# Optimization experiments

Measured on AMD Instinct MI355X. Metric: run time of the kernel, lower is better.

The kernel has to match this reference:

```python
import jax, jax.numpy as jnp
import numpy as np

EMBED = 512
H = 8
HD = EMBED // H           # 64
NUM_CLS = 4
WIN = 32                  # one-sided window radius
DIL = 1
WLEN = 2 * WIN + 1        # 65
CTX = NUM_CLS + WLEN      # 69
PATCH_LEN = 8192
B = 1
S = NUM_CLS + PATCH_LEN
THETA = 10000.0
COORD_HIGH = 100000.0
NEG = -1e30


def _rotate_half(x):
    # [..., x1, x2, ...] -> [..., -x2, x1, ...]
    x1 = x[..., 0::2]
    x2 = x[..., 1::2]
    return jnp.stack([-x2, x1], axis=-1).reshape(x.shape)


def _rope2d(x, coords):
    # x: (B,H,L,HD), coords: (B,L,2)
    half = HD // 2
    inv_freq = 1.0 / (THETA ** (jnp.arange(0, half, 2, dtype=jnp.float32) / half))  # (half//2,)
    xy = coords / COORD_HIGH
    fx = xy[..., 0][..., None] * inv_freq   # (B,L,half//2)
    fy = xy[..., 1][..., None] * inv_freq
    fx = jnp.repeat(fx, 2, axis=-1)         # (B,L,half)
    fy = jnp.repeat(fy, 2, axis=-1)
    freqs = jnp.concatenate([fx, fy], axis=-1)[:, None]  # (B,1,L,HD)
    return x * jnp.cos(freqs) + _rotate_half(x) * jnp.sin(freqs)


def setup_inputs() -> dict:
    key = jax.random.key(0)
    k1, k2, k3, k4, k5, k6 = jax.random.split(key, 6)
    x = jax.random.normal(k1, (B, S, EMBED), dtype=jnp.float32)
    coords = jax.random.uniform(k2, (B, PATCH_LEN, 2), dtype=jnp.float32) * COORD_HIGH
    sc = 1.0 / np.sqrt(EMBED)
    w_qkv = jax.random.normal(k3, (3 * EMBED, EMBED), dtype=jnp.float32) * sc
    b_qkv = jax.random.normal(k4, (3 * EMBED,), dtype=jnp.float32) * 0.02
    w_out = jax.random.normal(k5, (EMBED, EMBED), dtype=jnp.float32) * sc
    b_out = jax.random.normal(k6, (EMBED,), dtype=jnp.float32) * 0.02
    return {"x": x, "coords": coords, "w_qkv": w_qkv, "b_qkv": b_qkv,
            "w_out": w_out, "b_out": b_out}


def _forward(x, coords, w_qkv, b_qkv, w_out, b_out):
    Bb, seq_len, _ = x.shape
    qkv = x @ w_qkv.T + b_qkv                       # (B,S,3E)
    qkv = qkv.reshape(Bb, seq_len, 3, H, HD)
    qkv = jnp.transpose(qkv, (2, 0, 3, 1, 4))       # (3,B,H,S,HD)
    q, k, v = qkv[0], qkv[1], qkv[2]
    q_cls, k_cls, v_cls = q[:, :, :NUM_CLS], k[:, :, :NUM_CLS], v[:, :, :NUM_CLS]
    q_p, k_p, v_p = q[:, :, NUM_CLS:], k[:, :, NUM_CLS:], v[:, :, NUM_CLS:]

    q_p = _rope2d(q_p, coords)
    k_p = _rope2d(k_p, coords)
    k_all = jnp.concatenate([k_cls, k_p], axis=2)
    v_all = v

    scale = 1.0 / np.sqrt(HD)

    # --- global CLS attention: CLS queries attend to everything ---
    cls_scores = jnp.einsum('bhqd,bhkd->bhqk', q_cls, k_all) * scale
    cls_probs = jax.nn.softmax(cls_scores, axis=-1)
    cls_out = jnp.einsum('bhqk,bhkd->bhqd', cls_probs, v_all)

    # --- windowed patch attention: patch i -> [CLS | patches i-W..i+W (dilated)] ---
    L = PATCH_LEN
    pad = WIN * DIL
    k_pad = jnp.pad(k_p, ((0, 0), (0, 0), (pad, pad), (0, 0)))
    v_pad = jnp.pad(v_p, ((0, 0), (0, 0), (pad, pad), (0, 0)))
    gather_idx = jnp.arange(L)[:, None] + jnp.arange(WLEN)[None, :] * DIL  # (L,WLEN)
    k_win = k_pad[:, :, gather_idx]   # (B,H,L,WLEN,HD)
    v_win = v_pad[:, :, gather_idx]

    s_cls = jnp.einsum('bhld,bhcd->bhlc', q_p, k_cls) * scale     # (B,H,L,NUM_CLS)
    s_win = jnp.einsum('bhld,bhlwd->bhlw', q_p, k_win) * scale    # (B,H,L,WLEN)

    pos = jnp.arange(L)[:, None] + (jnp.arange(WLEN)[None, :] - WIN) * DIL
    in_bounds = (pos >= 0) & (pos < L)                            # (L,WLEN)
    s_win = jnp.where(in_bounds[None, None], s_win, NEG)

    scores = jnp.concatenate([s_cls, s_win], axis=-1)             # (B,H,L,CTX)
    probs = jax.nn.softmax(scores, axis=-1)
    p_cls, p_win = probs[..., :NUM_CLS], probs[..., NUM_CLS:]
    patch_out = (jnp.einsum('bhlc,bhcd->bhld', p_cls, v_cls)
                 + jnp.einsum('bhlw,bhlwd->bhld', p_win, v_win))

    out = jnp.concatenate([cls_out, patch_out], axis=2)           # (B,H,S,HD)
    out = jnp.transpose(out, (0, 2, 1, 3)).reshape(Bb, seq_len, EMBED)
    return out @ w_out.T + b_out


def reference(x, coords, w_qkv, b_qkv, w_out, b_out):
    return _forward(x, coords, w_qkv, b_qkv, w_out, b_out)
```

## Files before the change

kernel.cpp:

```cpp
#include <hip/hip_runtime.h>
#include <math.h>

#define EMBED 512
#define NHEAD 8
#define HD 64
#define NUM_CLS 4
#define WIN 32
#define WLEN 65
#define PATCH_LEN 8192
#define S_TOT 8196
#define QKV_LD 1536
#define VT_LD 8200

typedef short bf16x8 __attribute__((ext_vector_type(8)));
typedef float f32x4 __attribute__((ext_vector_type(4)));

__device__ __forceinline__ unsigned short f2bf(float f) {
    unsigned u = __float_as_uint(f);
    return (unsigned short)((u + 0x7fffu + ((u >> 16) & 1u)) >> 16);
}
__device__ __forceinline__ float bf2f(unsigned short v) {
    return __uint_as_float((unsigned)v << 16);
}

__global__ __launch_bounds__(256) void cast_all(const float* __restrict__ x,
                                                const float* __restrict__ wq,
                                                const float* __restrict__ wo,
                                                unsigned short* __restrict__ xb,
                                                unsigned short* __restrict__ wqb,
                                                unsigned short* __restrict__ wob)
{
    const int n1 = S_TOT * EMBED;
    const int n2 = 3 * EMBED * EMBED;
    const int n3 = EMBED * EMBED;
    const int i = (blockIdx.x * 256 + threadIdx.x) * 4;
    const float* src;
    unsigned short* dst;
    int j;
    if (i < n1)           { src = x;  dst = xb;  j = i; }
    else if (i < n1 + n2) { src = wq; dst = wqb; j = i - n1; }
    else if (i < n1 + n2 + n3) { src = wo; dst = wob; j = i - n1 - n2; }
    else return;
    const float4 v = *(const float4*)(src + j);
    ushort4 o;
    o.x = f2bf(v.x); o.y = f2bf(v.y); o.z = f2bf(v.z); o.w = f2bf(v.w);
    *(ushort4*)(dst + j) = o;
}

template <int MODE, typename OutT>
__global__ __launch_bounds__(256) void gemm_bf16_nt(const unsigned short* __restrict__ A,
                                                    const unsigned short* __restrict__ B,
                                                    const float* __restrict__ bias,
                                                    OutT* __restrict__ C,
                                                    int M, int N, int K,
                                                    const float* __restrict__ coords,
                                                    unsigned short* __restrict__ vT)
{
    __shared__ __align__(16) unsigned short As[128 * 32];
    __shared__ __align__(16) unsigned short Bs[128 * 32];
    const int tid = threadIdx.x;
    const int lane = tid & 63, w = tid >> 6;
    const int bn = blockIdx.x, bm = blockIdx.y;

    const int ar0 = tid >> 2;
    const int col8 = (tid & 3) * 8;
    int gm0 = bm * 128 + ar0;       if (gm0 >= M) gm0 = M - 1;
    int gm1 = bm * 128 + ar0 + 64;  if (gm1 >= M) gm1 = M - 1;
    const int gn0 = bn * 128 + ar0;
    const int gn1 = bn * 128 + ar0 + 64;
    const unsigned short* pa0 = A + (size_t)gm0 * K + col8;
    const unsigned short* pa1 = A + (size_t)gm1 * K + col8;
    const unsigned short* pb0 = B + (size_t)gn0 * K + col8;
    const unsigned short* pb1 = B + (size_t)gn1 * K + col8;
    unsigned short* la0 = As + tid * 8;
    unsigned short* la1 = As + (tid + 256) * 8;
    unsigned short* lb0 = Bs + tid * 8;
    unsigned short* lb1 = Bs + (tid + 256) * 8;

    const int wr = (w & 1) * 64;
    const int wc = (w >> 1) * 64;
    const int fr = lane & 15;
    const int fk = (lane >> 4) * 8;

    f32x4 acc[4][4];
#pragma unroll
    for (int mi = 0; mi < 4; ++mi)
#pragma unroll
        for (int ni = 0; ni < 4; ++ni) acc[mi][ni] = (f32x4)0.f;

    for (int k0 = 0; k0 < K; k0 += 32) {
        __builtin_amdgcn_global_load_lds((const __attribute__((address_space(1))) void*)(pa0 + k0),
                                         (__attribute__((address_space(3))) void*)la0, 16, 0, 0);
        __builtin_amdgcn_global_load_lds((const __attribute__((address_space(1))) void*)(pa1 + k0),
                                         (__attribute__((address_space(3))) void*)la1, 16, 0, 0);
        __builtin_amdgcn_global_load_lds((const __attribute__((address_space(1))) void*)(pb0 + k0),
                                         (__attribute__((address_space(3))) void*)lb0, 16, 0, 0);
        __builtin_amdgcn_global_load_lds((const __attribute__((address_space(1))) void*)(pb1 + k0),
                                         (__attribute__((address_space(3))) void*)lb1, 16, 0, 0);
        __syncthreads();

        bf16x8 af[4], bf[4];
#pragma unroll
        for (int mi = 0; mi < 4; ++mi)
            af[mi] = *(const bf16x8*)(As + (wr + mi * 16 + fr) * 32 + fk);
#pragma unroll
        for (int ni = 0; ni < 4; ++ni)
            bf[ni] = *(const bf16x8*)(Bs + (wc + ni * 16 + fr) * 32 + fk);
#pragma unroll
        for (int mi = 0; mi < 4; ++mi)
#pragma unroll
            for (int ni = 0; ni < 4; ++ni)
                acc[mi][ni] = __builtin_amdgcn_mfma_f32_16x16x32_bf16(af[mi], bf[ni], acc[mi][ni], 0, 0, 0);
        __syncthreads();
    }

    const int ccol = bn * 128 + wc + fr;

    if constexpr (MODE == 0) {
#pragma unroll
        for (int mi = 0; mi < 4; ++mi) {
            const int rbase = bm * 128 + wr + mi * 16 + (lane >> 4) * 4;
#pragma unroll
            for (int r = 0; r < 4; ++r) {
                const int row = rbase + r;
                if (row < M) {
#pragma unroll
                    for (int ni = 0; ni < 4; ++ni)
                        C[(size_t)row * N + ccol + ni * 16] = acc[mi][ni][r] + bias[ccol + ni * 16];
                }
            }
        }
    } else {
        __shared__ __align__(16) unsigned short EX[64 * 136];
        if (bn < 8) {
            ushort2* rt = (ushort2*)EX;
            for (int idx = tid; idx < 4096; idx += 256) {
                const int rr = idx >> 5, pr = idx & 31;
                int l = bm * 128 + rr - NUM_CLS;
                l = l < 0 ? 0 : (l > PATCH_LEN - 1 ? PATCH_LEN - 1 : l);
                const float cxy = coords[l * 2 + (pr >> 4)] * 1e-5f;
                const float f = cxy * __expf(-(float)(pr & 15) * 0.5756462732485114f);
                float sn, cs;
                __sincosf(f, &sn, &cs);
                ushort2 e; e.x = f2bf(cs); e.y = f2bf(sn);
                rt[idx] = e;
            }
            __syncthreads();
#pragma unroll
            for (int mi = 0; mi < 4; ++mi) {
                const int rloc0 = wr + mi * 16 + (lane >> 4) * 4;
#pragma unroll
                for (int r = 0; r < 4; ++r) {
                    const int rloc = rloc0 + r;
                    const int row = bm * 128 + rloc;
                    const bool patch = (row >= NUM_CLS) && (row < M);
#pragma unroll
                    for (int ni = 0; ni < 4; ++ni) {
                        const int col = ccol + ni * 16;
                        const float biased = acc[mi][ni][r] + bias[col];
                        const float prt = __shfl_xor(biased, 1);
                        float outv = biased;
                        if (patch) {
                            const ushort2 e = rt[rloc * 32 + ((col & 63) >> 1)];
                            const float cs = bf2f(e.x), sn = bf2f(e.y);
                            outv = (col & 1) ? (biased * cs + prt * sn)
                                             : (biased * cs - prt * sn);
                        }
                        if (row < M) C[(size_t)row * N + col] = (OutT)f2bf(outv);
                    }
                }
            }
        } else {
            const int dbase = (bn - 8) * 128;
#pragma unroll
            for (int mi = 0; mi < 4; ++mi) {
                const int rbase = bm * 128 + wr + mi * 16 + (lane >> 4) * 4;
#pragma unroll
                for (int ni = 0; ni < 4; ++ni) {
                    const int col = ccol + ni * 16;
#pragma unroll
                    for (int r = 0; r < 4; ++r) {
                        const int row = rbase + r;
                        if (row < M)
                            C[(size_t)row * N + col] = (OutT)f2bf(acc[mi][ni][r] + bias[col]);
                    }
                }
            }
            for (int p = 0; p < 2; ++p) {
                __syncthreads();
                if ((w >> 1) == p) {
#pragma unroll
                    for (int mi = 0; mi < 4; ++mi) {
                        const int tok0 = wr + mi * 16 + (lane >> 4) * 4;
                        const int rw = bm * 128 + tok0;
#pragma unroll
                        for (int ni = 0; ni < 4; ++ni) {
                            const int col = ccol + ni * 16;
                            const int dloc = fr + 16 * ni;
                            ushort4 o;
                            o.x = (rw + 0 < M) ? f2bf(acc[mi][ni][0] + bias[col]) : (unsigned short)0;
                            o.y = (rw + 1 < M) ? f2bf(acc[mi][ni][1] + bias[col]) : (unsigned short)0;
                            o.z = (rw + 2 < M) ? f2bf(acc[mi][ni][2] + bias[col]) : (unsigned short)0;
                            o.w = (rw + 3 < M) ? f2bf(acc[mi][ni][3] + bias[col]) : (unsigned short)0;
                            *(ushort4*)(EX + dloc * 136 + tok0) = o;
                        }
                    }
                }
                __syncthreads();
                const int d = tid >> 2;
                const int tch = (tid & 3) * 32;
                const int gtok = bm * 128 + tch;
                unsigned short* dst = vT + (size_t)(dbase + p * 64 + d) * VT_LD + gtok;
                const unsigned short* srcl = EX + d * 136 + tch;
                if (gtok + 32 <= VT_LD) {
#pragma unroll
                    for (int c2 = 0; c2 < 32; c2 += 8)
                        *(bf16x8*)(dst + c2) = *(const bf16x8*)(srcl + c2);
                } else {
                    for (int c2 = 0; c2 < 32; ++c2)
                        if (gtok + c2 < VT_LD) dst[c2] = srcl[c2];
                }
            }
        }
    }
}

#define CCH 128
#define NCHUNK ((S_TOT + CCH - 1) / CCH)
#define PSTRIDE 68

__global__ __launch_bounds__(256) void cls_attn_partial(const unsigned short* __restrict__ qkv,
                                                        float* __restrict__ part)
{
    const int h = blockIdx.x;
    const int c = blockIdx.y;
    const int tid = threadIdx.x;
    const int base = c * CCH;

    __shared__ float qs[4][64];
    __shared__ __align__(16) unsigned short Kl[128 * 64];
    __shared__ float sc[4][CCH];
    __shared__ float ored[4][4][64];
    __shared__ float ml[4][2];

    {
        const int qi = tid >> 6, d = tid & 63;
        qs[qi][d] = bf2f(qkv[(size_t)qi * QKV_LD + h * HD + d]);
    }
    for (int i = tid; i < 1024; i += 256) {
        const int kr = i >> 3;
        const int dc = (i & 7) ^ (kr & 7);
        int j = base + kr; if (j > S_TOT - 1) j = S_TOT - 1;
        const unsigned short* g = qkv + (size_t)j * QKV_LD + EMBED + h * HD + dc * 8;
        __builtin_amdgcn_global_load_lds((const __attribute__((address_space(1))) void*)g,
                                         (__attribute__((address_space(3))) void*)(Kl + i * 8), 16, 0, 0);
    }
    __syncthreads();

    {
        const int jj = tid & 127;
        const int qp = (tid >> 7) * 2;
        const int j = base + jj;
        float s0 = -INFINITY, s1 = -INFINITY;
        if (j < S_TOT) {
            float a0 = 0.f, a1 = 0.f;
#pragma unroll
            for (int cch = 0; cch < 8; ++cch) {
                const int slot = cch ^ (jj & 7);
                const bf16x8 kv8 = *(const bf16x8*)(Kl + jj * 64 + slot * 8);
#pragma unroll
                for (int u = 0; u < 8; ++u) {
                    const float kf = bf2f((unsigned short)kv8[u]);
                    a0 += qs[qp + 0][cch * 8 + u] * kf;
                    a1 += qs[qp + 1][cch * 8 + u] * kf;
                }
            }
            s0 = a0 * 0.125f; s1 = a1 * 0.125f;
        }
        sc[qp + 0][jj] = s0;
        sc[qp + 1][jj] = s1;
    }
    __syncthreads();

    const int w = tid >> 6, lane = tid & 63;
    {
        float m = fmaxf(sc[w][lane], sc[w][lane + 64]);
#pragma unroll
        for (int off = 32; off > 0; off >>= 1) m = fmaxf(m, __shfl_xor(m, off, 64));
        const float e0 = expf(sc[w][lane] - m);
        const float e1 = expf(sc[w][lane + 64] - m);
        sc[w][lane] = e0; sc[w][lane + 64] = e1;
        float lsum = e0 + e1;
#pragma unroll
        for (int off = 32; off > 0; off >>= 1) lsum += __shfl_xor(lsum, off, 64);
        if (lane == 0) { ml[w][0] = m; ml[w][1] = lsum; }
    }
    __syncthreads();

    {
        const int g = w, d = lane;
        float a0 = 0.f, a1 = 0.f, a2 = 0.f, a3 = 0.f;
        for (int jj = g; jj < CCH; jj += 4) {
            const int j = base + jj;
            if (j >= S_TOT) break;
            const float vv = bf2f(qkv[(size_t)j * QKV_LD + 2 * EMBED + h * HD + d]);
            a0 += sc[0][jj] * vv; a1 += sc[1][jj] * vv;
            a2 += sc[2][jj] * vv; a3 += sc[3][jj] * vv;
        }
        ored[g][0][d] = a0; ored[g][1][d] = a1; ored[g][2][d] = a2; ored[g][3][d] = a3;
    }
    __syncthreads();

    {
        const int qi = tid >> 6, d = tid & 63;
        const float o = ored[0][qi][d] + ored[1][qi][d] + ored[2][qi][d] + ored[3][qi][d];
        float* pb = part + ((size_t)(h * NCHUNK + c) * 4 + qi) * PSTRIDE;
        pb[d] = o;
        if (d == 0) { pb[64] = ml[qi][0]; pb[65] = ml[qi][1]; }
    }
}

__global__ __launch_bounds__(256) void cls_attn_combine(const float* __restrict__ part,
                                                        unsigned short* __restrict__ attn)
{
    const int h = blockIdx.x;
    const int qi = threadIdx.x >> 6, d = threadIdx.x & 63;
    float M = -INFINITY;
    for (int c = 0; c < NCHUNK; ++c)
        M = fmaxf(M, part[((size_t)(h * NCHUNK + c) * 4 + qi) * PSTRIDE + 64]);
    float acc = 0.f, L = 0.f;
    for (int c = 0; c < NCHUNK; ++c) {
        const float* pb = part + ((size_t)(h * NCHUNK + c) * 4 + qi) * PSTRIDE;
        const float s = expf(pb[64] - M);
        acc += s * pb[d];
        L   += s * pb[65];
    }
    attn[(size_t)qi * EMBED + h * HD + d] = f2bf(acc / L);
}

#define SW 116
#define PW 136

__global__ __launch_bounds__(256) void patch_attn_mfma(
    const unsigned short* __restrict__ qkv,
    const unsigned short* __restrict__ vT,
    unsigned short* __restrict__ attnb)
{
    const int l0 = blockIdx.x * 32;
    const int h = blockIdx.y;
    const int tid = threadIdx.x;
    const int lane = tid & 63, w = tid >> 6;

    __shared__ __align__(16) unsigned short Qs[32 * 64];
    __shared__ __align__(16) unsigned short Ks[112 * 64];
    __shared__ __align__(16) unsigned short Vt[64 * 128];
    __shared__ __align__(16) float Sm[32 * SW];

    {
        const int i = tid;
        const int t = i >> 3;
        const int dcl = (i & 7) ^ (t & 7);
        const unsigned short* g = qkv + (size_t)(NUM_CLS + l0 + t) * QKV_LD + h * HD + dcl * 8;
        __builtin_amdgcn_global_load_lds((const __attribute__((address_space(1))) void*)g,
                                         (__attribute__((address_space(3))) void*)(Qs + i * 8), 16, 0, 0);
    }
    for (int i = tid; i < 896; i += 256) {
        const int c = i >> 3;
        const int dcl = (i & 7) ^ (c & 7);
        int tok = (c >= 104 && c < 108) ? (c - 104) : (l0 - 32 + c);
        tok = tok < 0 ? 0 : (tok > S_TOT - 1 ? S_TOT - 1 : tok);
        const unsigned short* g = qkv + (size_t)tok * QKV_LD + EMBED + h * HD + dcl * 8;
        __builtin_amdgcn_global_load_lds((const __attribute__((address_space(1))) void*)g,
                                         (__attribute__((address_space(3))) void*)(Ks + i * 8), 16, 0, 0);
    }
    for (int i = tid; i < 1024; i += 256) {
        const int d = i >> 4;
        const int kcl = (i & 15) ^ (d & 15);
        const int c0 = kcl * 8;
        int tokb = (c0 == 104) ? 0 : (l0 - 32 + c0);
        tokb = tokb < 0 ? 0 : (tokb > 8192 ? 8192 : tokb);
        const unsigned short* g = vT + (size_t)(h * HD + d) * VT_LD + tokb;
        __builtin_amdgcn_global_load_lds((const __attribute__((address_space(1))) void*)g,
                                         (__attribute__((address_space(3))) void*)(Vt + i * 8), 16, 0, 0);
    }
    __syncthreads();

    bf16x8 qf[2][2];
#pragma unroll
    for (int mt = 0; mt < 2; ++mt)
#pragma unroll
        for (int ks = 0; ks < 2; ++ks) {
            const int row = mt * 16 + (lane & 15);
            const int dc = (ks * 4 + (lane >> 4)) ^ (row & 7);
            qf[mt][ks] = *(const bf16x8*)(Qs + row * 64 + dc * 8);
        }
    for (int idx = w; idx < 14; idx += 4) {
        const int mt = idx & 1, nt = idx >> 1;
        f32x4 acc = (f32x4)0.f;
#pragma unroll
        for (int ks = 0; ks < 2; ++ks) {
            const int kr = nt * 16 + (lane & 15);
            const int dc = (ks * 4 + (lane >> 4)) ^ (kr & 7);
            const bf16x8 kf = *(const bf16x8*)(Ks + kr * 64 + dc * 8);
            acc = __builtin_amdgcn_mfma_f32_16x16x32_bf16(qf[mt][ks], kf, acc, 0, 0, 0);
        }
        const int col = nt * 16 + (lane & 15);
        const int r0 = mt * 16 + (lane >> 4) * 4;
#pragma unroll
        for (int r = 0; r < 4; ++r) Sm[(r0 + r) * SW + col] = acc[r];
    }
    __syncthreads();

    {
        const int t = tid >> 3, lq = tid & 7;
        float e[14];
        float m = -INFINITY;
#pragma unroll
        for (int j = 0; j < 14; ++j) {
            const int c = lq + 8 * j;
            bool valid;
            if (c >= 104) valid = (c < 108);
            else {
                const int r = c - 4;
                const int pos = l0 - 32 + r;
                valid = (c >= 4) && (c < 100) && (r >= t) && (r <= t + 64) &&
                        (pos >= 0) && (pos < PATCH_LEN);
            }
            e[j] = valid ? Sm[t * SW + c] * 0.125f : -INFINITY;
            m = fmaxf(m, e[j]);
        }
#pragma unroll
        for (int off = 1; off < 8; off <<= 1) m = fmaxf(m, __shfl_xor(m, off, 64));
        float sum = 0.f;
#pragma unroll
        for (int j = 0; j < 14; ++j) { e[j] = expf(e[j] - m); sum += e[j]; }
#pragma unroll
        for (int off = 1; off < 8; off <<= 1) sum += __shfl_xor(sum, off, 64);
        const float inv = 1.f / sum;
        __syncthreads();
        unsigned short* P = (unsigned short*)Sm;
#pragma unroll
        for (int j = 0; j < 14; ++j) P[t * PW + lq + 8 * j] = f2bf(e[j] * inv);
        ushort2 z; z.x = 0; z.y = 0;
        *(ushort2*)(P + (tid >> 3) * PW + 112 + (tid & 7) * 2) = z;
    }
    __syncthreads();

    {
        const unsigned short* P = (const unsigned short*)Sm;
        const int mt = w & 1;
        bf16x8 pf[4];
#pragma unroll
        for (int ks = 0; ks < 4; ++ks) {
            const int row = mt * 16 + (lane & 15);
            pf[ks] = *(const bf16x8*)(P + row * PW + ks * 32 + (lane >> 4) * 8);
        }
#pragma unroll
        for (int nn = 0; nn < 2; ++nn) {
            const int nt = (w >> 1) + nn * 2;
            f32x4 acc = (f32x4)0.f;
#pragma unroll
            for (int ks = 0; ks < 4; ++ks) {
                const int d = nt * 16 + (lane & 15);
                const int kc = (ks * 4 + (lane >> 4)) ^ (d & 15);
                const bf16x8 vf = *(const bf16x8*)(Vt + d * 128 + kc * 8);
                acc = __builtin_amdgcn_mfma_f32_16x16x32_bf16(pf[ks], vf, acc, 0, 0, 0);
            }
            const int dcol = nt * 16 + (lane & 15);
            const int r0 = mt * 16 + (lane >> 4) * 4;
#pragma unroll
            for (int r = 0; r < 4; ++r)
                attnb[(size_t)(NUM_CLS + l0 + r0 + r) * EMBED + h * HD + dcol] = f2bf(acc[r]);
        }
    }
}

extern "C" void kernel_launch(void* const* d_in, const int* in_sizes, int n_in,
                              void* d_out, int out_size, void* d_ws, size_t ws_size,
                              hipStream_t stream)
{
    const float* x      = (const float*)d_in[0];
    const float* coords = (const float*)d_in[1];
    const float* w_qkv  = (const float*)d_in[2];
    const float* b_qkv  = (const float*)d_in[3];
    const float* w_out  = (const float*)d_in[4];
    const float* b_out  = (const float*)d_in[5];
    float* out = (float*)d_out;

    char* p = (char*)d_ws;
    unsigned short* qkv   = (unsigned short*)p;  p += (size_t)S_TOT * QKV_LD * 2;
    unsigned short* vT    = (unsigned short*)p;  p += (size_t)EMBED * VT_LD * 2;
    unsigned short* attnb = (unsigned short*)p;  p += (size_t)S_TOT * EMBED * 2;
    float*          part  = (float*)p;           p += (size_t)NHEAD * NCHUNK * 4 * PSTRIDE * 4;
    unsigned short* wob   = (unsigned short*)p;  p += (size_t)EMBED * EMBED * 2;
    unsigned short* xb    = (unsigned short*)p;  p += (size_t)S_TOT * EMBED * 2;
    unsigned short* wqb   = (unsigned short*)p;


    {
        const int total = S_TOT * EMBED + 3 * EMBED * EMBED + EMBED * EMBED;
        cast_all<<<(total / 4 + 255) / 256, 256, 0, stream>>>(x, w_qkv, w_out, xb, wqb, wob);
    }

    gemm_bf16_nt<1, unsigned short><<<dim3((3 * EMBED) / 128, (S_TOT + 127) / 128), 256, 0, stream>>>(
        xb, wqb, b_qkv, qkv, S_TOT, 3 * EMBED, EMBED, coords, vT);

    cls_attn_partial<<<dim3(NHEAD, NCHUNK), 256, 0, stream>>>(qkv, part);
    cls_attn_combine<<<NHEAD, 256, 0, stream>>>(part, attnb);

    patch_attn_mfma<<<dim3(PATCH_LEN / 32, NHEAD), 256, 0, stream>>>(qkv, vT, attnb);

    gemm_bf16_nt<0, float><<<dim3(EMBED / 128, (S_TOT + 127) / 128), 256, 0, stream>>>(
        attnb, wob, b_out, out, S_TOT, EMBED, EMBED, nullptr, nullptr);
}
```

Measured before the change: 195.6 us.

## Double-buffer GEMM LDS tiles, stage QKV epilogue stores, shrink output GEMM tile

Splits the templated GEMM into a QKV kernel and an output-projection kernel. Both now double-buffer the A/B tiles in LDS so the next K-slice loads while the current one feeds the MFMAs, with one barrier per iteration instead of two. The Q/K RoPE epilogue packs bf16 results and stages them through LDS so rows are written with 16-byte coalesced stores instead of scattered 2-byte stores. The output GEMM uses 64-row tiles, doubling block count for better CU occupancy, at the cost of more LDS per block and more B-tile reloads.

```diff
diff --git a/kernel.cpp b/kernel.cpp
--- a/kernel.cpp
+++ b/kernel.cpp
@@ -21,6 +21,10 @@
 }
 __device__ __forceinline__ float bf2f(unsigned short v) {
     return __uint_as_float((unsigned)v << 16);
+}
+__device__ __forceinline__ void gll16(const unsigned short* g, unsigned short* l) {
+    __builtin_amdgcn_global_load_lds((const __attribute__((address_space(1))) void*)g,
+                                     (__attribute__((address_space(3))) void*)l, 16, 0, 0);
 }
 
 __global__ __launch_bounds__(256) void cast_all(const float* __restrict__ x,
@@ -47,17 +51,18 @@
     *(ushort4*)(dst + j) = o;
 }
 
-template <int MODE, typename OutT>
-__global__ __launch_bounds__(256) void gemm_bf16_nt(const unsigned short* __restrict__ A,
-                                                    const unsigned short* __restrict__ B,
-                                                    const float* __restrict__ bias,
-                                                    OutT* __restrict__ C,
-                                                    int M, int N, int K,
-                                                    const float* __restrict__ coords,
-                                                    unsigned short* __restrict__ vT)
-{
-    __shared__ __align__(16) unsigned short As[128 * 32];
-    __shared__ __align__(16) unsigned short Bs[128 * 32];
+#define EXW 136
+__global__ __launch_bounds__(256) void gemm_qkv(const unsigned short* __restrict__ A,
+                                                const unsigned short* __restrict__ B,
+                                                const float* __restrict__ bias,
+                                                unsigned short* __restrict__ C,
+                                                const float* __restrict__ coords,
+                                                unsigned short* __restrict__ vT)
+{
+    const int M = S_TOT, N = 3 * EMBED, K = EMBED;
+    __shared__ __align__(16) unsigned short As[2][128 * 32];
+    __shared__ __align__(16) unsigned short Bs[2][128 * 32];
+    __shared__ __align__(16) unsigned short EX[64 * EXW];
     const int tid = threadIdx.x;
     const int lane = tid & 63, w = tid >> 6;
     const int bn = blockIdx.x, bm = blockIdx.y;
@@ -66,16 +71,10 @@
     const int col8 = (tid & 3) * 8;
     int gm0 = bm * 128 + ar0;       if (gm0 >= M) gm0 = M - 1;
     int gm1 = bm * 128 + ar0 + 64;  if (gm1 >= M) gm1 = M - 1;
-    const int gn0 = bn * 128 + ar0;
-    const int gn1 = bn * 128 + ar0 + 64;
     const unsigned short* pa0 = A + (size_t)gm0 * K + col8;
     const unsigned short* pa1 = A + (size_t)gm1 * K + col8;
-    const unsigned short* pb0 = B + (size_t)gn0 * K + col8;
-    const unsigned short* pb1 = B + (size_t)gn1 * K + col8;
-    unsigned short* la0 = As + tid * 8;
-    unsigned short* la1 = As + (tid + 256) * 8;
-    unsigned short* lb0 = Bs + tid * 8;
-    unsigned short* lb1 = Bs + (tid + 256) * 8;
+    const unsigned short* pb0 = B + (size_t)(bn * 128 + ar0) * K + col8;
+    const unsigned short* pb1 = B + (size_t)(bn * 128 + ar0 + 64) * K + col8;
 
     const int wr = (w & 1) * 64;
     const int wc = (w >> 1) * 64;
@@ -88,138 +87,230 @@
 #pragma unroll
         for (int ni = 0; ni < 4; ++ni) acc[mi][ni] = (f32x4)0.f;
 
-    for (int k0 = 0; k0 < K; k0 += 32) {
-        __builtin_amdgcn_global_load_lds((const __attribute__((address_space(1))) void*)(pa0 + k0),
-                                         (__attribute__((address_space(3))) void*)la0, 16, 0, 0);
-        __builtin_amdgcn_global_load_lds((const __attribute__((address_space(1))) void*)(pa1 + k0),
-                                         (__attribute__((address_space(3))) void*)la1, 16, 0, 0);
-        __builtin_amdgcn_global_load_lds((const __attribute__((address_space(1))) void*)(pb0 + k0),
-                                         (__attribute__((address_space(3))) void*)lb0, 16, 0, 0);
-        __builtin_amdgcn_global_load_lds((const __attribute__((address_space(1))) void*)(pb1 + k0),
-                                         (__attribute__((address_space(3))) void*)lb1, 16, 0, 0);
+    gll16(pa0, As[0] + tid * 8);
+    gll16(pa1, As[0] + (tid + 256) * 8);
+    gll16(pb0, Bs[0] + tid * 8);
+    gll16(pb1, Bs[0] + (tid + 256) * 8);
+
+    for (int it = 0; it < 16; ++it) {
         __syncthreads();
-
+        if (it + 1 < 16) {
+            const int k0 = (it + 1) * 32;
+            const int nb = (it + 1) & 1;
+            gll16(pa0 + k0, As[nb] + tid * 8);
+            gll16(pa1 + k0, As[nb] + (tid + 256) * 8);
+            gll16(pb0 + k0, Bs[nb] + tid * 8);
+            gll16(pb1 + k0, Bs[nb] + (tid + 256) * 8);
+        }
+        const int cb = it & 1;
         bf16x8 af[4], bf[4];
 #pragma unroll
         for (int mi = 0; mi < 4; ++mi)
-            af[mi] = *(const bf16x8*)(As + (wr + mi * 16 + fr) * 32 + fk);
+            af[mi] = *(const bf16x8*)(As[cb] + (wr + mi * 16 + fr) * 32 + fk);
 #pragma unroll
         for (int ni = 0; ni < 4; ++ni)
-            bf[ni] = *(const bf16x8*)(Bs + (wc + ni * 16 + fr) * 32 + fk);
+            bf[ni] = *(const bf16x8*)(Bs[cb] + (wc + ni * 16 + fr) * 32 + fk);
 #pragma unroll
         for (int mi = 0; mi < 4; ++mi)
 #pragma unroll
             for (int ni = 0; ni < 4; ++ni)
                 acc[mi][ni] = __builtin_amdgcn_mfma_f32_16x16x32_bf16(af[mi], bf[ni], acc[mi][ni], 0, 0, 0);
+    }
+
+    const int ccol = bn * 128 + wc + fr;
+
+    if (bn < 8) {
+        ushort2* rt = (ushort2*)EX;
+        for (int idx = tid; idx < 4096; idx += 256) {
+            const int rr = idx >> 5, pr = idx & 31;
+            int l = bm * 128 + rr - NUM_CLS;
+            l = l < 0 ? 0 : (l > PATCH_LEN - 1 ? PATCH_LEN - 1 : l);
+            const float cxy = coords[l * 2 + (pr >> 4)] * 1e-5f;
+            const float f = cxy * __expf(-(float)(pr & 15) * 0.5756462732485114f);
+            float sn, cs;
+            __sincosf(f, &sn, &cs);
+            ushort2 e; e.x = f2bf(cs); e.y = f2bf(sn);
+            rt[idx] = e;
+        }
         __syncthreads();
-    }
-
-    const int ccol = bn * 128 + wc + fr;
-
-    if constexpr (MODE == 0) {
+
+        unsigned pv[4][4][2];
 #pragma unroll
         for (int mi = 0; mi < 4; ++mi) {
-            const int rbase = bm * 128 + wr + mi * 16 + (lane >> 4) * 4;
 #pragma unroll
             for (int r = 0; r < 4; ++r) {
-                const int row = rbase + r;
-                if (row < M) {
-#pragma unroll
-                    for (int ni = 0; ni < 4; ++ni)
-                        C[(size_t)row * N + ccol + ni * 16] = acc[mi][ni][r] + bias[ccol + ni * 16];
-                }
-            }
-        }
-    } else {
-        __shared__ __align__(16) unsigned short EX[64 * 136];
-        if (bn < 8) {
-            ushort2* rt = (ushort2*)EX;
-            for (int idx = tid; idx < 4096; idx += 256) {
-                const int rr = idx >> 5, pr = idx & 31;
-                int l = bm * 128 + rr - NUM_CLS;
-                l = l < 0 ? 0 : (l > PATCH_LEN - 1 ? PATCH_LEN - 1 : l);
-                const float cxy = coords[l * 2 + (pr >> 4)] * 1e-5f;
-                const float f = cxy * __expf(-(float)(pr & 15) * 0.5756462732485114f);
-                float sn, cs;
-                __sincosf(f, &sn, &cs);
-                ushort2 e; e.x = f2bf(cs); e.y = f2bf(sn);
-                rt[idx] = e;
-            }
-            __syncthreads();
-#pragma unroll
-            for (int mi = 0; mi < 4; ++mi) {
-                const int rloc0 = wr + mi * 16 + (lane >> 4) * 4;
-#pragma unroll
-                for (int r = 0; r < 4; ++r) {
-                    const int rloc = rloc0 + r;
-                    const int row = bm * 128 + rloc;
-                    const bool patch = (row >= NUM_CLS) && (row < M);
-#pragma unroll
-                    for (int ni = 0; ni < 4; ++ni) {
-                        const int col = ccol + ni * 16;
-                        const float biased = acc[mi][ni][r] + bias[col];
-                        const float prt = __shfl_xor(biased, 1);
-                        float outv = biased;
-                        if (patch) {
-                            const ushort2 e = rt[rloc * 32 + ((col & 63) >> 1)];
-                            const float cs = bf2f(e.x), sn = bf2f(e.y);
-                            outv = (col & 1) ? (biased * cs + prt * sn)
-                                             : (biased * cs - prt * sn);
-                        }
-                        if (row < M) C[(size_t)row * N + col] = (OutT)f2bf(outv);
-                    }
-                }
-            }
-        } else {
-            const int dbase = (bn - 8) * 128;
-#pragma unroll
-            for (int mi = 0; mi < 4; ++mi) {
-                const int rbase = bm * 128 + wr + mi * 16 + (lane >> 4) * 4;
+                const int rloc = wr + mi * 16 + (lane >> 4) * 4 + r;
+                const int row = bm * 128 + rloc;
+                const bool patch = (row >= NUM_CLS) && (row < M);
 #pragma unroll
                 for (int ni = 0; ni < 4; ++ni) {
                     const int col = ccol + ni * 16;
+                    const float biased = acc[mi][ni][r] + bias[col];
+                    const float prt = __shfl_xor(biased, 1);
+                    float outv = biased;
+                    if (patch) {
+                        const ushort2 e = rt[rloc * 32 + ((col & 63) >> 1)];
+                        const float cs = bf2f(e.x), sn = bf2f(e.y);
+                        outv = (col & 1) ? (biased * cs + prt * sn)
+                                         : (biased * cs - prt * sn);
+                    }
+                    const unsigned us = f2bf(outv);
+                    if (r & 1) pv[mi][ni][r >> 1] |= us << 16;
+                    else       pv[mi][ni][r >> 1] = us;
+                }
+            }
+        }
+        for (int p = 0; p < 2; ++p) {
+            __syncthreads();
+            if ((w & 1) == p) {
+#pragma unroll
+                for (int mi = 0; mi < 4; ++mi) {
 #pragma unroll
                     for (int r = 0; r < 4; ++r) {
-                        const int row = rbase + r;
-                        if (row < M)
-                            C[(size_t)row * N + col] = (OutT)f2bf(acc[mi][ni][r] + bias[col]);
-                    }
-                }
-            }
-            for (int p = 0; p < 2; ++p) {
-                __syncthreads();
-                if ((w >> 1) == p) {
-#pragma unroll
-                    for (int mi = 0; mi < 4; ++mi) {
-                        const int tok0 = wr + mi * 16 + (lane >> 4) * 4;
-                        const int rw = bm * 128 + tok0;
+                        const int rl = mi * 16 + (lane >> 4) * 4 + r;
 #pragma unroll
                         for (int ni = 0; ni < 4; ++ni) {
-                            const int col = ccol + ni * 16;
-                            const int dloc = fr + 16 * ni;
-                            ushort4 o;
-                            o.x = (rw + 0 < M) ? f2bf(acc[mi][ni][0] + bias[col]) : (unsigned short)0;
-                            o.y = (rw + 1 < M) ? f2bf(acc[mi][ni][1] + bias[col]) : (unsigned short)0;
-                            o.z = (rw + 2 < M) ? f2bf(acc[mi][ni][2] + bias[col]) : (unsigned short)0;
-                            o.w = (rw + 3 < M) ? f2bf(acc[mi][ni][3] + bias[col]) : (unsigned short)0;
-                            *(ushort4*)(EX + dloc * 136 + tok0) = o;
+                            const unsigned pw = pv[mi][ni][r >> 1];
+                            EX[rl * EXW + wc + fr + ni * 16] =
+                                (unsigned short)((r & 1) ? (pw >> 16) : (pw & 0xffff));
                         }
                     }
                 }
-                __syncthreads();
-                const int d = tid >> 2;
-                const int tch = (tid & 3) * 32;
-                const int gtok = bm * 128 + tch;
-                unsigned short* dst = vT + (size_t)(dbase + p * 64 + d) * VT_LD + gtok;
-                const unsigned short* srcl = EX + d * 136 + tch;
-                if (gtok + 32 <= VT_LD) {
-#pragma unroll
-                    for (int c2 = 0; c2 < 32; c2 += 8)
-                        *(bf16x8*)(dst + c2) = *(const bf16x8*)(srcl + c2);
-                } else {
-                    for (int c2 = 0; c2 < 32; ++c2)
-                        if (gtok + c2 < VT_LD) dst[c2] = srcl[c2];
+            }
+            __syncthreads();
+#pragma unroll
+            for (int i = 0; i < 4; ++i) {
+                const int idx = tid + 256 * i;
+                const int rowl = idx >> 4, ch = idx & 15;
+                const int grow = bm * 128 + p * 64 + rowl;
+                if (grow < M)
+                    *(bf16x8*)(C + (size_t)grow * N + bn * 128 + ch * 8) =
+                        *(const bf16x8*)(EX + rowl * EXW + ch * 8);
+            }
+        }
+    } else {
+        const int dbase = (bn - 8) * 128;
+#pragma unroll
+        for (int mi = 0; mi < 4; ++mi) {
+            const int rbase = bm * 128 + wr + mi * 16 + (lane >> 4) * 4;
+#pragma unroll
+            for (int ni = 0; ni < 4; ++ni) {
+                const int col = ccol + ni * 16;
+#pragma unroll
+                for (int r = 0; r < 4; ++r) {
+                    const int row = rbase + r;
+                    if (row < M)
+                        C[(size_t)row * N + col] = f2bf(acc[mi][ni][r] + bias[col]);
                 }
+            }
+        }
+        for (int p = 0; p < 2; ++p) {
+            __syncthreads();
+            if ((w >> 1) == p) {
+#pragma unroll
+                for (int mi = 0; mi < 4; ++mi) {
+                    const int tok0 = wr + mi * 16 + (lane >> 4) * 4;
+                    const int rw = bm * 128 + tok0;
+#pragma unroll
+                    for (int ni = 0; ni < 4; ++ni) {
+                        const int col = ccol + ni * 16;
+                        const int dloc = fr + 16 * ni;
+                        ushort4 o;
+                        o.x = (rw + 0 < M) ? f2bf(acc[mi][ni][0] + bias[col]) : (unsigned short)0;
+                        o.y = (rw + 1 < M) ? f2bf(acc[mi][ni][1] + bias[col]) : (unsigned short)0;
+                        o.z = (rw + 2 < M) ? f2bf(acc[mi][ni][2] + bias[col]) : (unsigned short)0;
+                        o.w = (rw + 3 < M) ? f2bf(acc[mi][ni][3] + bias[col]) : (unsigned short)0;
+                        *(ushort4*)(EX + dloc * EXW + tok0) = o;
+                    }
+                }
+            }
+            __syncthreads();
+            const int d = tid >> 2;
+            const int tch = (tid & 3) * 32;
+            const int gtok = bm * 128 + tch;
+            unsigned short* dst = vT + (size_t)(dbase + p * 64 + d) * VT_LD + gtok;
+            const unsigned short* srcl = EX + d * EXW + tch;
+            if (gtok + 32 <= VT_LD) {
+#pragma unroll
+                for (int c2 = 0; c2 < 32; c2 += 8)
+                    *(bf16x8*)(dst + c2) = *(const bf16x8*)(srcl + c2);
+            } else {
+                for (int c2 = 0; c2 < 32; ++c2)
+                    if (gtok + c2 < VT_LD) dst[c2] = srcl[c2];
+            }
+        }
+    }
+}
+
+__global__ __launch_bounds__(256) void gemm_out(const unsigned short* __restrict__ A,
+                                                const unsigned short* __restrict__ B,
+                                                const float* __restrict__ bias,
+                                                float* __restrict__ C)
+{
+    const int M = S_TOT, N = EMBED, K = EMBED;
+    __shared__ __align__(16) unsigned short As[2][64 * 32];
+    __shared__ __align__(16) unsigned short Bs[2][128 * 32];
+    const int tid = threadIdx.x;
+    const int lane = tid & 63, w = tid >> 6;
+    const int bn = blockIdx.x, bm = blockIdx.y;
+
+    const int ar0 = tid >> 2;
+    const int col8 = (tid & 3) * 8;
+    int gm0 = bm * 64 + ar0;  if (gm0 >= M) gm0 = M - 1;
+    const unsigned short* pa0 = A + (size_t)gm0 * K + col8;
+    const unsigned short* pb0 = B + (size_t)(bn * 128 + ar0) * K + col8;
+    const unsigned short* pb1 = B + (size_t)(bn * 128 + ar0 + 64) * K + col8;
+
+    const int wr = (w & 1) * 32;
+    const int wc = (w >> 1) * 64;
+    const int fr = lane & 15;
+    const int fk = (lane >> 4) * 8;
+
+    f32x4 acc[2][4];
+#pragma unroll
+    for (int mi = 0; mi < 2; ++mi)
+#pragma unroll
+        for (int ni = 0; ni < 4; ++ni) acc[mi][ni] = (f32x4)0.f;
+
+    gll16(pa0, As[0] + tid * 8);
+    gll16(pb0, Bs[0] + tid * 8);
+    gll16(pb1, Bs[0] + (tid + 256) * 8);
+
+    for (int it = 0; it < 16; ++it) {
+        __syncthreads();
+        if (it + 1 < 16) {
+            const int k0 = (it + 1) * 32;
+            const int nb = (it + 1) & 1;
+            gll16(pa0 + k0, As[nb] + tid * 8);
+            gll16(pb0 + k0, Bs[nb] + tid * 8);
+            gll16(pb1 + k0, Bs[nb] + (tid + 256) * 8);
+        }
+        const int cb = it & 1;
+        bf16x8 af[2], bf[4];
+#pragma unroll
+        for (int mi = 0; mi < 2; ++mi)
+            af[mi] = *(const bf16x8*)(As[cb] + (wr + mi * 16 + fr) * 32 + fk);
+#pragma unroll
+        for (int ni = 0; ni < 4; ++ni)
+            bf[ni] = *(const bf16x8*)(Bs[cb] + (wc + ni * 16 + fr) * 32 + fk);
+#pragma unroll
+        for (int mi = 0; mi < 2; ++mi)
+#pragma unroll
+            for (int ni = 0; ni < 4; ++ni)
+                acc[mi][ni] = __builtin_amdgcn_mfma_f32_16x16x32_bf16(af[mi], bf[ni], acc[mi][ni], 0, 0, 0);
+    }
+
+    const int ccol = bn * 128 + wc + fr;
+#pragma unroll
+    for (int mi = 0; mi < 2; ++mi) {
+        const int rbase = bm * 64 + wr + mi * 16 + (lane >> 4) * 4;
+#pragma unroll
+        for (int r = 0; r < 4; ++r) {
+            const int row = rbase + r;
+            if (row < M) {
+#pragma unroll
+                for (int ni = 0; ni < 4; ++ni)
+                    C[(size_t)row * N + ccol + ni * 16] = acc[mi][ni][r] + bias[ccol + ni * 16];
             }
         }
     }
@@ -251,9 +342,7 @@
         const int kr = i >> 3;
         const int dc = (i & 7) ^ (kr & 7);
         int j = base + kr; if (j > S_TOT - 1) j = S_TOT - 1;
-        const unsigned short* g = qkv + (size_t)j * QKV_LD + EMBED + h * HD + dc * 8;
-        __builtin_amdgcn_global_load_lds((const __attribute__((address_space(1))) void*)g,
-                                         (__attribute__((address_space(3))) void*)(Kl + i * 8), 16, 0, 0);
+        gll16(qkv + (size_t)j * QKV_LD + EMBED + h * HD + dc * 8, Kl + i * 8);
     }
     __syncthreads();
 
@@ -360,18 +449,14 @@
         const int i = tid;
         const int t = i >> 3;
         const int dcl = (i & 7) ^ (t & 7);
-        const unsigned short* g = qkv + (size_t)(NUM_CLS + l0 + t) * QKV_LD + h * HD + dcl * 8;
-        __builtin_amdgcn_global_load_lds((const __attribute__((address_space(1))) void*)g,
-                                         (__attribute__((address_space(3))) void*)(Qs + i * 8), 16, 0, 0);
+        gll16(qkv + (size_t)(NUM_CLS + l0 + t) * QKV_LD + h * HD + dcl * 8, Qs + i * 8);
     }
     for (int i = tid; i < 896; i += 256) {
         const int c = i >> 3;
         const int dcl = (i & 7) ^ (c & 7);
         int tok = (c >= 104 && c < 108) ? (c - 104) : (l0 - 32 + c);
         tok = tok < 0 ? 0 : (tok > S_TOT - 1 ? S_TOT - 1 : tok);
-        const unsigned short* g = qkv + (size_t)tok * QKV_LD + EMBED + h * HD + dcl * 8;
-        __builtin_amdgcn_global_load_lds((const __attribute__((address_space(1))) void*)g,
-                                         (__attribute__((address_space(3))) void*)(Ks + i * 8), 16, 0, 0);
+        gll16(qkv + (size_t)tok * QKV_LD + EMBED + h * HD + dcl * 8, Ks + i * 8);
     }
     for (int i = tid; i < 1024; i += 256) {
         const int d = i >> 4;
@@ -379,9 +464,7 @@
         const int c0 = kcl * 8;
         int tokb = (c0 == 104) ? 0 : (l0 - 32 + c0);
         tokb = tokb < 0 ? 0 : (tokb > 8192 ? 8192 : tokb);
-        const unsigned short* g = vT + (size_t)(h * HD + d) * VT_LD + tokb;
-        __builtin_amdgcn_global_load_lds((const __attribute__((address_space(1))) void*)g,
-                                         (__attribute__((address_space(3))) void*)(Vt + i * 8), 16, 0, 0);
+        gll16(vT + (size_t)(h * HD + d) * VT_LD + tokb, Vt + i * 8);
     }
     __syncthreads();
 
@@ -502,14 +585,12 @@
         cast_all<<<(total / 4 + 255) / 256, 256, 0, stream>>>(x, w_qkv, w_out, xb, wqb, wob);
     }
 
-    gemm_bf16_nt<1, unsigned short><<<dim3((3 * EMBED) / 128, (S_TOT + 127) / 128), 256, 0, stream>>>(
-        xb, wqb, b_qkv, qkv, S_TOT, 3 * EMBED, EMBED, coords, vT);
+    gemm_qkv<<<dim3(12, 65), 256, 0, stream>>>(xb, wqb, b_qkv, qkv, coords, vT);
 
     cls_attn_partial<<<dim3(NHEAD, NCHUNK), 256, 0, stream>>>(qkv, part);
     cls_attn_combine<<<NHEAD, 256, 0, stream>>>(part, attnb);
 
     patch_attn_mfma<<<dim3(PATCH_LEN / 32, NHEAD), 256, 0, stream>>>(qkv, vT, attnb);
 
-    gemm_bf16_nt<0, float><<<dim3(EMBED / 128, (S_TOT + 127) / 128), 256, 0, stream>>>(
-        attnb, wob, b_out, out, S_TOT, EMBED, EMBED, nullptr, nullptr);
-}
+    gemm_out<<<dim3(4, 129), 256, 0, stream>>>(attnb, wob, b_out, out);
+}
```

Result: no change. 194.0 us (-0.8%).
